# Kernel tuning notes

Measured on AMD Instinct MI355X. Metric: run time of the kernel, lower is better.

Reference implementation:

```python
import jax, jax.numpy as jnp
import numpy as np

N_NODES = 100000
N_EDGES = 3200000
D_IN = 128
D_OUT = 128


def setup_inputs() -> dict:
    key = jax.random.key(0)
    k1, k2, k3, k4, k5 = jax.random.split(key, 5)
    x = jax.random.normal(k1, (N_NODES, D_IN), dtype=jnp.float32)
    adj_rows = jax.random.randint(k2, (N_EDGES,), 0, N_NODES, dtype=jnp.int64)
    adj_cols = jax.random.randint(k3, (N_EDGES,), 0, N_NODES, dtype=jnp.int64)
    adj_vals = jax.random.uniform(k4, (N_EDGES,), dtype=jnp.float32)
    # torch Linear weight has shape (dim_out, dim_in)
    W = jax.random.normal(k5, (D_OUT, D_IN), dtype=jnp.float32) * (1.0 / np.sqrt(D_IN))
    return {"x": x, "adj_rows": adj_rows, "adj_cols": adj_cols, "adj_vals": adj_vals, "W": W}


def reference(x, adj_rows, adj_cols, adj_vals, W):
    # h = Linear(x) with no bias: x @ W^T  -> [N, D_OUT]
    h = x @ W.T
    # sparse.mm(adjacency, h): out[r] = sum_e vals[e] * h[cols[e]] for edges with rows[e]==r
    msgs = adj_vals[:, None] * h[adj_cols]           # [E, D_OUT]
    agg = jax.ops.segment_sum(msgs, adj_rows, num_segments=N_NODES)
    return jax.nn.relu(agg)
```

## Files before the change

kernel.cpp:

```cpp
#include <hip/hip_runtime.h>
#include <stdint.h>

typedef unsigned short u16;
typedef unsigned int u32;
typedef unsigned long long u64;
typedef __attribute__((ext_vector_type(8))) short short8;
typedef __attribute__((ext_vector_type(4))) float floatx4;

#define DIM 128
#define DIM2 64
#define NBK 1792
#define NBK_PT 7
#define NB_SH 6
#define AGG_NB 64
#define AGG_CAP 2560
#define SC_C 12800
#define NSEG 256

__device__ __forceinline__ u32 f32_to_bf16_rne(float f) {
  u32 u = __float_as_uint(f);
  u32 r = u + 0x7fffu + ((u >> 16) & 1u);
  return r >> 16;
}
__device__ __forceinline__ float bf16_to_f32(u32 u) { return __uint_as_float(u << 16); }
__device__ __forceinline__ u32 pack2bf16(float a, float b) {
  return f32_to_bf16_rne(a) | (f32_to_bf16_rne(b) << 16);
}

union FragU {
  u32 d[4];
  short8 s;
};

__global__ __launch_bounds__(256) void gemm_mfma(const float* __restrict__ x,
                                                 const float* __restrict__ W,
                                                 u16* __restrict__ h, int N) {
  __shared__ u32 Wl[DIM * DIM2];
  int tid = threadIdx.x;
#pragma unroll
  for (int i = 0; i < 8; ++i) {
    int ga = tid + 256 * i;
    int o = ga >> 4, g = ga & 15;
    const float* src = W + (size_t)o * DIM + g * 8;
    floatx4 f0 = *(const floatx4*)src;
    floatx4 f1 = *(const floatx4*)(src + 4);
    int slot = (g + o) & 15;
    u32* dst = &Wl[o * DIM2 + slot * 4];
    dst[0] = pack2bf16(f0.x, f0.y);
    dst[1] = pack2bf16(f0.z, f0.w);
    dst[2] = pack2bf16(f1.x, f1.y);
    dst[3] = pack2bf16(f1.z, f1.w);
  }
  __syncthreads();

  int lane = tid & 63;
  int wave = tid >> 6;
  int m = lane & 15;
  int kg = lane >> 4;
  int ntile = (N + 63) >> 6;

  for (int t = blockIdx.x; t < ntile; t += 256) {
    int nodeBase = t * 64 + wave * 16;
    if (nodeBase >= N) continue;

    short8 a[4];
    const float* xr = x + (size_t)(nodeBase + m) * DIM + kg * 8;
#pragma unroll
    for (int kt = 0; kt < 4; ++kt) {
      floatx4 f0 = *(const floatx4*)(xr + kt * 32);
      floatx4 f1 = *(const floatx4*)(xr + kt * 32 + 4);
      FragU fu;
      fu.d[0] = pack2bf16(f0.x, f0.y);
      fu.d[1] = pack2bf16(f0.z, f0.w);
      fu.d[2] = pack2bf16(f1.x, f1.y);
      fu.d[3] = pack2bf16(f1.z, f1.w);
      a[kt] = fu.s;
    }

#pragma unroll
    for (int ot = 0; ot < 8; ++ot) {
      int o = ot * 16 + m;
      floatx4 acc = {0.f, 0.f, 0.f, 0.f};
#pragma unroll
      for (int kt = 0; kt < 4; ++kt) {
        int slot = (kt * 4 + kg + o) & 15;
        short8 b = *(short8*)&Wl[o * DIM2 + slot * 4];
        acc = __builtin_amdgcn_mfma_f32_16x16x32_bf16(a[kt], b, acc, 0, 0, 0);
      }
#pragma unroll
      for (int r = 0; r < 4; ++r) {
        int node = nodeBase + kg * 4 + r;
        h[(size_t)node * DIM + ot * 16 + m] = (u16)f32_to_bf16_rne(acc[r]);
      }
    }
  }
}

__device__ __forceinline__ void scan_nbk(u32* cnt, u32* excl, u32* wtot) {
  int tid = threadIdx.x, lane = tid & 63, wave = tid >> 6;
  u32 c[NBK_PT], sum = 0;
#pragma unroll
  for (int k = 0; k < NBK_PT; ++k) {
    c[k] = cnt[tid * NBK_PT + k];
    sum += c[k];
  }
  u32 inc = sum;
#pragma unroll
  for (int d = 1; d < 64; d <<= 1) {
    u32 t = __shfl_up(inc, d, 64);
    if (lane >= d) inc += t;
  }
  if (lane == 63) wtot[wave] = inc;
  __syncthreads();
  u32 wbase = 0;
  for (int w = 0; w < wave; ++w) wbase += wtot[w];
  u32 run = wbase + inc - sum;
#pragma unroll
  for (int k = 0; k < NBK_PT; ++k) {
    excl[tid * NBK_PT + k] = run;
    run += c[k];
  }
  __syncthreads();
}

__global__ __launch_bounds__(256) void sort_scatter(const int* __restrict__ rows,
                                                    const int* __restrict__ cols,
                                                    const float* __restrict__ vals,
                                                    u32* __restrict__ bcol,
                                                    u16* __restrict__ bval,
                                                    u32* __restrict__ dirT, int E, int B,
                                                    int nsc) {
  __shared__ u32 hist[NBK];
  __shared__ u32 starts[NBK];
  __shared__ u32 wtot[4];
  __shared__ u32 s_lo[SC_C];
  __shared__ u16 s_val[SC_C];
  int tid = threadIdx.x;
  int wg = blockIdx.x;
  int base = wg * SC_C;
  int tot = min(SC_C, E - base);

  for (int b = tid; b < NBK; b += 256) hist[b] = 0;
  __syncthreads();
  for (int j = tid; j < tot; j += 256) {
    atomicAdd(&hist[((u32)rows[base + j]) >> NB_SH], 1u);
  }
  __syncthreads();
  scan_nbk(hist, starts, wtot);
  for (int b = tid; b < NBK; b += 256) hist[b] = starts[b];
  __syncthreads();
  for (int j = tid; j < tot; j += 256) {
    u32 r = (u32)rows[base + j];
    u32 bk = r >> NB_SH;
    u32 p = atomicAdd(&hist[bk], 1u);
    s_lo[p] = ((r & 63u) << 26) | ((u32)cols[base + j] << 8);
    s_val[p] = (u16)f32_to_bf16_rne(vals[base + j]);
  }
  __syncthreads();
  for (int i = tid; i < tot; i += 256) {
    bcol[(size_t)base + i] = s_lo[i];
    bval[(size_t)base + i] = s_val[i];
  }
  for (int b = tid; b < B; b += 256) {
    dirT[(size_t)b * nsc + wg] = (starts[b] << 16) | (hist[b] - starts[b]);
  }
}

__global__ __launch_bounds__(256) void agg_bucket(const u32* __restrict__ bcol,
                                                  const u16* __restrict__ bval,
                                                  const u32* __restrict__ dirT,
                                                  const u32* __restrict__ h,
                                                  float* __restrict__ out, int N,
                                                  int nsc, int B) {
  __shared__ u64 s_rec[AGG_CAP];
  __shared__ u16 map[AGG_CAP];
  __shared__ u32 segdir[NSEG], segdst[NSEG];
  __shared__ u32 cnt[AGG_NB], excl[AGG_NB], ptr[AGG_NB];
  __shared__ u32 sT;
  int tid = threadIdx.x, lane = tid & 63, wave = tid >> 6;
  int b = blockIdx.x;
  int nodeBase = b << NB_SH;
  int lane4 = lane * 4;
  const char* hb = (const char*)h;

  for (int w = tid; w < NSEG; w += 256)
    segdir[w] = (w < nsc) ? dirT[(size_t)b * nsc + w] : 0u;
  if (tid < AGG_NB) cnt[tid] = 0;
  __syncthreads();
  if (tid < 64) {
    u32 c[4], sum = 0;
#pragma unroll
    for (int k = 0; k < 4; ++k) {
      c[k] = segdir[lane * 4 + k] & 0xffffu;
      sum += c[k];
    }
    u32 inc = sum;
#pragma unroll
    for (int d = 1; d < 64; d <<= 1) {
      u32 t = __shfl_up(inc, d, 64);
      if (lane >= d) inc += t;
    }
    u32 run = inc - sum;
#pragma unroll
    for (int k = 0; k < 4; ++k) {
      segdst[lane * 4 + k] = run;
      run += c[k];
    }
    if (lane == 63) sT = inc;
  }
  __syncthreads();
  int T = (int)sT;

  if (T <= AGG_CAP) {
    for (int w = tid; w < nsc; w += 256) {
      u32 dv = segdir[w];
      u32 c = dv & 0xffffu;
      u32 d0 = segdst[w];
      for (u32 i = 0; i < c; ++i) map[d0 + i] = (u16)w;
    }
    __syncthreads();
    u32 rlo[10], rv[10];
#pragma unroll
    for (int k = 0; k < 10; ++k) {
      int g = tid + 256 * k;
      rlo[k] = 0;
      rv[k] = 0;
      if (g < T) {
        int w = map[g];
        u32 dv = segdir[w];
        u32 src = (u32)w * SC_C + (dv >> 16) + ((u32)g - segdst[w]);
        rlo[k] = bcol[src];
        rv[k] = bval[src];
        atomicAdd(&cnt[rlo[k] >> 26], 1u);
      }
    }
    __syncthreads();
    if (tid < 64) {
      u32 c = cnt[tid], inc = c;
#pragma unroll
      for (int d = 1; d < 64; d <<= 1) {
        u32 t = __shfl_up(inc, d, 64);
        if (lane >= d) inc += t;
      }
      excl[tid] = inc - c;
      ptr[tid] = inc - c;
    }
    __syncthreads();
#pragma unroll
    for (int k = 0; k < 10; ++k) {
      int g = tid + 256 * k;
      if (g < T) {
        u32 p = atomicAdd(&ptr[rlo[k] >> 26], 1u);
        s_rec[p] = ((u64)(rv[k] << 16) << 32) | rlo[k];
      }
    }
    __syncthreads();
    int wbeg = (int)excl[wave * 16];
    int wend = (int)ptr[wave * 16 + 15];
    float a0 = 0.f, a1 = 0.f;
    int curn = -1;
    for (int e = wbeg; e < wend; e += 8) {
      u32 lo8[8];
      float v8[8];
      u32 hd[8];
#pragma unroll
      for (int g = 0; g < 8; ++g) {
        int ee = e + g;
        bool act = ee < wend;
        u64 r = s_rec[act ? ee : (wend - 1)];
        lo8[g] = (u32)r;
        v8[g] = act ? __uint_as_float((u32)(r >> 32)) : 0.f;
      }
#pragma unroll
      for (int g = 0; g < 8; ++g) {
        hd[g] = *(const u32*)(hb + ((lo8[g] & 0x01FFFF00u) + lane4));
      }
#pragma unroll
      for (int g = 0; g < 8; ++g) {
        int nid = __builtin_amdgcn_readfirstlane((int)(lo8[g] >> 26));
        if (nid != curn) {
          if (curn >= 0) {
            float2 o = make_float2(fmaxf(a0, 0.f), fmaxf(a1, 0.f));
            *(float2*)(out + (size_t)(nodeBase + curn) * DIM + 2 * lane) = o;
          }
          curn = nid;
          a0 = 0.f;
          a1 = 0.f;
        }
        float v = v8[g];
        a0 += v * bf16_to_f32(hd[g] & 0xffffu);
        a1 += v * bf16_to_f32(hd[g] >> 16);
      }
    }
    if (curn >= 0) {
      float2 o = make_float2(fmaxf(a0, 0.f), fmaxf(a1, 0.f));
      *(float2*)(out + (size_t)(nodeBase + curn) * DIM + 2 * lane) = o;
    }
    for (int nn = 0; nn < 16; ++nn) {
      int nl = wave * 16 + nn;
      int node = nodeBase + nl;
      if (cnt[nl] == 0 && node < N) {
        *(float2*)(out + (size_t)node * DIM + 2 * lane) = make_float2(0.f, 0.f);
      }
    }
  } else {
    for (int nn = 0; nn < 16; ++nn) {
      int nl = wave * 16 + nn;
      int node = nodeBase + nl;
      if (node >= N) continue;
      float a0 = 0.f, a1 = 0.f;
      for (int w = 0; w < nsc; ++w) {
        u32 dv = segdir[w];
        int sc = (int)(dv & 0xffffu);
        u32 so = dv >> 16;
        for (int r = 0; r < sc; ++r) {
          u32 lo = bcol[(size_t)w * SC_C + so + r];
          if ((int)(lo >> 26) == nl) {
            u32 d = *(const u32*)(hb + ((lo & 0x01FFFF00u) + lane4));
            float v = bf16_to_f32(bval[(size_t)w * SC_C + so + r]);
            a0 += v * bf16_to_f32(d & 0xffffu);
            a1 += v * bf16_to_f32(d >> 16);
          }
        }
      }
      *(float2*)(out + (size_t)node * DIM + 2 * lane) =
          make_float2(fmaxf(a0, 0.f), fmaxf(a1, 0.f));
    }
  }
}

extern "C" void kernel_launch(void* const* d_in, const int* in_sizes, int n_in,
                              void* d_out, int out_size, void* d_ws, size_t ws_size,
                              hipStream_t stream) {
  const float* x    = (const float*)d_in[0];
  const int*   rows = (const int*)d_in[1];
  const int*   cols = (const int*)d_in[2];
  const float* vals = (const float*)d_in[3];
  const float* W    = (const float*)d_in[4];

  const int N = in_sizes[0] / DIM;
  const int E = in_sizes[1];
  const int B = (N + AGG_NB - 1) / AGG_NB;
  const int nsc = (E + SC_C - 1) / SC_C;

  char* wsb = (char*)d_ws;
  size_t o = 0;
  u16* h = (u16*)wsb;            o += (size_t)N * DIM * sizeof(u16);
  u32* bcol = (u32*)(wsb + o);   o += (size_t)nsc * SC_C * sizeof(u32);
  u16* bval = (u16*)(wsb + o);   o += (size_t)nsc * SC_C * sizeof(u16);
  u32* dirT = (u32*)(wsb + o);   o += (size_t)B * nsc * sizeof(u32);

  gemm_mfma<<<256, 256, 0, stream>>>(x, W, h, N);
  sort_scatter<<<nsc, 256, 0, stream>>>(rows, cols, vals, bcol, bval, dirT, E, B, nsc);
  agg_bucket<<<B, 256, 0, stream>>>(bcol, bval, dirT, (const u32*)h,
                                    (float*)d_out, N, nsc, B);
}
```

Measured before the change: 345.4 us.

## Scatter sorted edges directly to global, widen sort blocks, drop agg map table

The sort kernel now runs 1024-thread blocks and writes each edge straight to its bucketed global position instead of staging in shared memory and copying out, which removes the large LDS staging arrays and one pass. The histogram scan is folded into a two-per-thread inline scan. In the aggregation kernel the per-element segment map is replaced by a per-thread contiguous chunk with a binary search plus a forward walk, and records are kept as separate u32/u16 arrays, cutting LDS use and a serial fill loop. The cost is scattered, uncoalesced global writes in the sort kernel and less coalesced gathers in the aggregation kernel.

```diff
diff --git a/kernel.cpp b/kernel.cpp
--- a/kernel.cpp
+++ b/kernel.cpp
@@ -10,7 +10,6 @@
 #define DIM 128
 #define DIM2 64
 #define NBK 1792
-#define NBK_PT 7
 #define NB_SH 6
 #define AGG_NB 64
 #define AGG_CAP 2560
@@ -96,72 +95,61 @@
   }
 }
 
-__device__ __forceinline__ void scan_nbk(u32* cnt, u32* excl, u32* wtot) {
-  int tid = threadIdx.x, lane = tid & 63, wave = tid >> 6;
-  u32 c[NBK_PT], sum = 0;
-#pragma unroll
-  for (int k = 0; k < NBK_PT; ++k) {
-    c[k] = cnt[tid * NBK_PT + k];
-    sum += c[k];
-  }
-  u32 inc = sum;
-#pragma unroll
-  for (int d = 1; d < 64; d <<= 1) {
-    u32 t = __shfl_up(inc, d, 64);
-    if (lane >= d) inc += t;
-  }
-  if (lane == 63) wtot[wave] = inc;
-  __syncthreads();
-  u32 wbase = 0;
-  for (int w = 0; w < wave; ++w) wbase += wtot[w];
-  u32 run = wbase + inc - sum;
-#pragma unroll
-  for (int k = 0; k < NBK_PT; ++k) {
-    excl[tid * NBK_PT + k] = run;
-    run += c[k];
-  }
-  __syncthreads();
-}
-
-__global__ __launch_bounds__(256) void sort_scatter(const int* __restrict__ rows,
-                                                    const int* __restrict__ cols,
-                                                    const float* __restrict__ vals,
-                                                    u32* __restrict__ bcol,
-                                                    u16* __restrict__ bval,
-                                                    u32* __restrict__ dirT, int E, int B,
-                                                    int nsc) {
+__global__ __launch_bounds__(1024) void sort_scatter(const int* __restrict__ rows,
+                                                     const int* __restrict__ cols,
+                                                     const float* __restrict__ vals,
+                                                     u32* __restrict__ bcol,
+                                                     u16* __restrict__ bval,
+                                                     u32* __restrict__ dirT, int E, int B,
+                                                     int nsc) {
   __shared__ u32 hist[NBK];
   __shared__ u32 starts[NBK];
-  __shared__ u32 wtot[4];
-  __shared__ u32 s_lo[SC_C];
-  __shared__ u16 s_val[SC_C];
-  int tid = threadIdx.x;
+  __shared__ u32 wtot[16];
+  int tid = threadIdx.x, lane = tid & 63, wv = tid >> 6;
   int wg = blockIdx.x;
   int base = wg * SC_C;
   int tot = min(SC_C, E - base);
 
-  for (int b = tid; b < NBK; b += 256) hist[b] = 0;
-  __syncthreads();
-  for (int j = tid; j < tot; j += 256) {
+  for (int b = tid; b < NBK; b += 1024) hist[b] = 0;
+  __syncthreads();
+  for (int j = tid; j < tot; j += 1024) {
     atomicAdd(&hist[((u32)rows[base + j]) >> NB_SH], 1u);
   }
   __syncthreads();
-  scan_nbk(hist, starts, wtot);
-  for (int b = tid; b < NBK; b += 256) hist[b] = starts[b];
-  __syncthreads();
-  for (int j = tid; j < tot; j += 256) {
+  {
+    int i0 = tid * 2;
+    u32 c0 = (i0 < NBK) ? hist[i0] : 0u;
+    u32 c1 = (i0 + 1 < NBK) ? hist[i0 + 1] : 0u;
+    u32 sum = c0 + c1, inc = sum;
+#pragma unroll
+    for (int d = 1; d < 64; d <<= 1) {
+      u32 t = __shfl_up(inc, d, 64);
+      if (lane >= d) inc += t;
+    }
+    if (lane == 63) wtot[wv] = inc;
+    __syncthreads();
+    u32 wbase = 0;
+    for (int w = 0; w < wv; ++w) wbase += wtot[w];
+    u32 ex = wbase + inc - sum;
+    if (i0 < NBK) {
+      starts[i0] = ex;
+      hist[i0] = ex;
+    }
+    if (i0 + 1 < NBK) {
+      starts[i0 + 1] = ex + c0;
+      hist[i0 + 1] = ex + c0;
+    }
+    __syncthreads();
+  }
+  for (int j = tid; j < tot; j += 1024) {
     u32 r = (u32)rows[base + j];
     u32 bk = r >> NB_SH;
     u32 p = atomicAdd(&hist[bk], 1u);
-    s_lo[p] = ((r & 63u) << 26) | ((u32)cols[base + j] << 8);
-    s_val[p] = (u16)f32_to_bf16_rne(vals[base + j]);
-  }
-  __syncthreads();
-  for (int i = tid; i < tot; i += 256) {
-    bcol[(size_t)base + i] = s_lo[i];
-    bval[(size_t)base + i] = s_val[i];
-  }
-  for (int b = tid; b < B; b += 256) {
+    bcol[(size_t)base + p] = ((r & 63u) << 26) | ((u32)cols[base + j] << 8);
+    bval[(size_t)base + p] = (u16)f32_to_bf16_rne(vals[base + j]);
+  }
+  __syncthreads();
+  for (int b = tid; b < B; b += 1024) {
     dirT[(size_t)b * nsc + wg] = (starts[b] << 16) | (hist[b] - starts[b]);
   }
 }
@@ -172,8 +160,8 @@
                                                   const u32* __restrict__ h,
                                                   float* __restrict__ out, int N,
                                                   int nsc, int B) {
-  __shared__ u64 s_rec[AGG_CAP];
-  __shared__ u16 map[AGG_CAP];
+  __shared__ u32 s_lo[AGG_CAP];
+  __shared__ u16 s_v[AGG_CAP];
   __shared__ u32 segdir[NSEG], segdst[NSEG];
   __shared__ u32 cnt[AGG_NB], excl[AGG_NB], ptr[AGG_NB];
   __shared__ u32 sT;
@@ -212,23 +200,35 @@
   int T = (int)sT;
 
   if (T <= AGG_CAP) {
-    for (int w = tid; w < nsc; w += 256) {
-      u32 dv = segdir[w];
-      u32 c = dv & 0xffffu;
-      u32 d0 = segdst[w];
-      for (u32 i = 0; i < c; ++i) map[d0 + i] = (u16)w;
-    }
-    __syncthreads();
+    int npt = (T + 255) >> 8;
+    int g0 = tid * npt;
+    int gend = min(g0 + npt, T);
     u32 rlo[10], rv[10];
+    int sw = 0;
+    u32 swst = 0, swcnt = 0;
+    if (g0 < T) {
+      int lo = 0, hi = NSEG - 1;
+#pragma unroll
+      for (int s = 0; s < 8; ++s) {
+        int mid = (lo + hi + 1) >> 1;
+        if (segdst[mid] <= (u32)g0) lo = mid; else hi = mid - 1;
+      }
+      sw = lo;
+      swst = segdst[sw];
+      swcnt = segdir[sw] & 0xffffu;
+    }
 #pragma unroll
     for (int k = 0; k < 10; ++k) {
-      int g = tid + 256 * k;
       rlo[k] = 0;
       rv[k] = 0;
-      if (g < T) {
-        int w = map[g];
-        u32 dv = segdir[w];
-        u32 src = (u32)w * SC_C + (dv >> 16) + ((u32)g - segdst[w]);
+      int g = g0 + k;
+      if (g < gend) {
+        while ((u32)g >= swst + swcnt) {
+          ++sw;
+          swst = segdst[sw];
+          swcnt = segdir[sw] & 0xffffu;
+        }
+        u32 src = (u32)sw * SC_C + (segdir[sw] >> 16) + ((u32)g - swst);
         rlo[k] = bcol[src];
         rv[k] = bval[src];
         atomicAdd(&cnt[rlo[k] >> 26], 1u);
@@ -248,10 +248,11 @@
     __syncthreads();
 #pragma unroll
     for (int k = 0; k < 10; ++k) {
-      int g = tid + 256 * k;
-      if (g < T) {
+      int g = g0 + k;
+      if (g < gend) {
         u32 p = atomicAdd(&ptr[rlo[k] >> 26], 1u);
-        s_rec[p] = ((u64)(rv[k] << 16) << 32) | rlo[k];
+        s_lo[p] = rlo[k];
+        s_v[p] = (u16)rv[k];
       }
     }
     __syncthreads();
@@ -267,9 +268,9 @@
       for (int g = 0; g < 8; ++g) {
         int ee = e + g;
         bool act = ee < wend;
-        u64 r = s_rec[act ? ee : (wend - 1)];
-        lo8[g] = (u32)r;
-        v8[g] = act ? __uint_as_float((u32)(r >> 32)) : 0.f;
+        int idx = act ? ee : (wend - 1);
+        lo8[g] = s_lo[idx];
+        v8[g] = act ? bf16_to_f32((u32)s_v[idx]) : 0.f;
       }
 #pragma unroll
       for (int g = 0; g < 8; ++g) {
@@ -351,7 +352,7 @@
   u32* dirT = (u32*)(wsb + o);   o += (size_t)B * nsc * sizeof(u32);
 
   gemm_mfma<<<256, 256, 0, stream>>>(x, W, h, N);
-  sort_scatter<<<nsc, 256, 0, stream>>>(rows, cols, vals, bcol, bval, dirT, E, B, nsc);
+  sort_scatter<<<nsc, 1024, 0, stream>>>(rows, cols, vals, bcol, bval, dirT, E, B, nsc);
   agg_bucket<<<B, 256, 0, stream>>>(bcol, bval, dirT, (const u32*)h,
                                     (float*)d_out, N, nsc, B);
 }
```

New measurement: 439.2 us. +27.1%, slower.
